# Optimization experiments

Hardware: AMD Instinct MI355X
Metric: run time of the kernel (lower is better)

## Reference

```python
import jax, jax.numpy as jnp
import numpy as np

BIN_AGG = 16  # binAgg in source
K = 3         # forward-default im2col/col2im kernel size


def _im2col(x, k):
    # torch Im2Col (unfold), pad=0, stride=1, dilation=1
    B, C, H, W = x.shape
    oh, ow = H - k + 1, W - k + 1
    patches = [x[:, :, i:i + oh, j:j + ow] for i in range(k) for j in range(k)]
    cols = jnp.stack(patches, axis=2)            # [B, C, k*k, oh, ow]
    return cols.reshape(B, C * k * k, oh * ow)   # [B, C*k*k, L]


def _col2im(cols, k, H, W):
    # torch Col2Im (fold): overlap-add of patches back to [B, C, H, W]
    B, CK, L = cols.shape
    C = CK // (k * k)
    oh = H - k + 1
    cols = cols.reshape(B, C, k, k, oh, oh)
    img = jnp.zeros((B, C, H, W), cols.dtype)
    for i in range(k):
        for j in range(k):
            img = img.at[:, :, i:i + oh, j:j + oh].add(cols[:, :, i, j])
    return img


def bin_active(x):
    # sign(x) scaled by block-wise mean of |x| over blocks of 16 along last dim
    B, Kd, L = x.shape
    blocks = jnp.abs(x).reshape(B, Kd, L // BIN_AGG, BIN_AGG)
    scale = jnp.mean(blocks, axis=-1, keepdims=True)
    scale = jnp.broadcast_to(scale, blocks.shape).reshape(B, Kd, L)
    return scale * jnp.sign(x)


def setup_inputs() -> dict:
    key = jax.random.key(0)
    ks = jax.random.split(key, 5)
    B, Cin, Cout, H = 8, 64, 128, 130
    x = jax.random.normal(ks[0], (B, Cin, H, H), jnp.float32)
    gamma = 1.0 + 0.1 * jax.random.normal(ks[1], (Cin,), jnp.float32)
    beta = 0.1 * jax.random.normal(ks[2], (Cin,), jnp.float32)
    conv_w = 0.05 * jax.random.normal(ks[3], (Cout, Cin, 3, 3), jnp.float32)
    conv_b = 0.05 * jax.random.normal(ks[4], (Cout,), jnp.float32)
    return {"x": x, "gamma": gamma, "beta": beta, "conv_w": conv_w, "conv_b": conv_b}


def reference(x, gamma, beta, conv_w, conv_b):
    eps = 1e-4  # BatchNorm2d eps in source
    # BatchNorm2d (training-mode batch statistics, affine)
    mean = jnp.mean(x, axis=(0, 2, 3), keepdims=True)
    var = jnp.var(x, axis=(0, 2, 3), keepdims=True)
    xbn = (x - mean) * jax.lax.rsqrt(var + eps) * gamma[None, :, None, None] + beta[None, :, None, None]
    H = x.shape[2]
    cols = _im2col(xbn, K)          # [B, C*9, (H-2)^2]
    cols = bin_active(cols)         # block-mean binary quantization
    img = _col2im(cols, K, H, H)    # [B, C, H, W]
    y = jax.lax.conv_general_dilated(
        img, conv_w, window_strides=(1, 1), padding=((1, 1), (1, 1)),
        dimension_numbers=("NCHW", "OIHW", "NCHW"))
    y = y + conv_b[None, :, None, None]
    return jax.nn.relu(y)
```

## Files before the change

### kernel.cpp

```cpp
#include <hip/hip_runtime.h>
#include <math.h>

#define B_    8
#define CIN   64
#define COUT  128
#define H_    130
#define NPIX  (H_*H_)
#define NPX   (B_*NPIX)
#define IMW   132
#define ROWE  (8*IMW*8)

typedef __attribute__((ext_vector_type(8))) short short8;
typedef __attribute__((ext_vector_type(4))) float f32x4;

__device__ __forceinline__ ushort f2bf(float f) {
    uint u = __builtin_bit_cast(uint, f);
    uint r = (u + 0x7FFFu + ((u >> 16) & 1u)) >> 16;
    return (ushort)r;
}

__global__ __launch_bounds__(256) void bn_stage1(
    const float* __restrict__ x, float* __restrict__ part)
{
    const int c = blockIdx.x, b = blockIdx.y, tid = threadIdx.x;
    const float4* p = (const float4*)(x + ((size_t)b*CIN + c)*NPIX);
    float s = 0.f, q = 0.f;
    for (int i = tid; i < NPIX/4; i += 256) {
        float4 v = p[i];
        s += v.x + v.y + v.z + v.w;
        q += v.x*v.x + v.y*v.y + v.z*v.z + v.w*v.w;
    }
    #pragma unroll
    for (int off = 32; off; off >>= 1) { s += __shfl_down(s, off); q += __shfl_down(q, off); }
    __shared__ float ss[4], qq[4];
    if ((tid & 63) == 0) { ss[tid >> 6] = s; qq[tid >> 6] = q; }
    __syncthreads();
    if (tid == 0) {
        s = ss[0] + ss[1] + ss[2] + ss[3];
        q = qq[0] + qq[1] + qq[2] + qq[3];
        part[(c*B_ + b)*2]     = s;
        part[(c*B_ + b)*2 + 1] = q;
    }
}

__global__ void bn_stage2(
    const float* __restrict__ part, const float* __restrict__ gamma,
    const float* __restrict__ beta, float* __restrict__ abuf, float* __restrict__ bbuf)
{
    int c = threadIdx.x;
    float s = 0.f, q = 0.f;
    for (int b = 0; b < B_; ++b) { s += part[(c*B_+b)*2]; q += part[(c*B_+b)*2+1]; }
    float mean = s * (1.0f/135200.f);
    float var  = q * (1.0f/135200.f) - mean*mean;
    float a = gamma[c] / sqrtf(var + 1e-4f);
    abuf[c] = a;
    bbuf[c] = beta[c] - mean * a;
}

__global__ __launch_bounds__(256) void wprep(
    const float* __restrict__ w, ushort* __restrict__ wT)
{
    int i = blockIdx.x*256 + threadIdx.x;
    int co = i / 576, k = i - co*576;
    int dydx = k >> 6, ci = k & 63;
    wT[i] = f2bf(w[co*576 + ci*9 + dydx]);
}

__global__ __launch_bounds__(256) void binfold(
    const float* __restrict__ x, const float* __restrict__ abuf,
    const float* __restrict__ bbuf, ushort* __restrict__ img)
{
    __shared__ __align__(16) ushort tile[H_*66];
    __shared__ float absrow[4][132];
    __shared__ float wsum[4][24];
    const int yy = blockIdx.x;
    const int b  = blockIdx.y;
    const int tid = threadIdx.x, wv = tid >> 6, lane = tid & 63;
    uint* rowU = (uint*)(img + (size_t)(b*IMW + yy)*ROWE);

    if (yy == 0 || yy == IMW-1) {
        for (int i = tid; i < ROWE/2; i += 256) rowU[i] = 0u;
        return;
    }
    const int y = yy - 1;
    const float county = (float)min(min(y + 1, 3), H_ - y);

    for (int it = 0; it < 16; ++it) {
        const int ci = wv*16 + it;
        const float* row = x + (((size_t)b*CIN + ci)*H_ + y)*H_;
        const float a = abuf[ci], bb = bbuf[ci];
        float v0 = a*row[lane]      + bb;
        float v1 = a*row[lane + 64] + bb;
        float v2 = 0.f;
        if (lane < 2) v2 = a*row[lane + 128] + bb;
        absrow[wv][lane]      = fabsf(v0);
        absrow[wv][lane + 64] = fabsf(v1);
        if (lane < 2) absrow[wv][lane + 128] = fabsf(v2);
        asm volatile("s_waitcnt lgkmcnt(0)" ::: "memory");
        if (lane < 24) {
            int j = lane >> 3, bx = lane & 7;
            int s = j + bx*16;
            float acc = 0.f;
            #pragma unroll
            for (int t = 0; t < 16; ++t) acc += absrow[wv][s + t];
            wsum[wv][j*8 + bx] = acc;
        }
        asm volatile("s_waitcnt lgkmcnt(0)" ::: "memory");
        #pragma unroll
        for (int rep = 0; rep < 3; ++rep) {
            int xp = lane + rep*64;
            if (xp < H_) {
                float v = (rep == 0) ? v0 : (rep == 1) ? v1 : v2;
                float sgn = (v > 0.f) ? 1.f : ((v < 0.f) ? -1.f : 0.f);
                float sum = 0.f;
                #pragma unroll
                for (int j = 0; j < 3; ++j) {
                    int ox = xp - j;
                    if ((unsigned)ox < 128u) sum += wsum[wv][j*8 + (ox >> 4)];
                }
                tile[xp*66 + ci] = f2bf(sgn * county * sum * 0.0625f);
            }
        }
    }
    __syncthreads();
    const uint* tU = (const uint*)tile;
    for (int i = tid; i < 8*H_*4; i += 256) {
        int cg = (int)((unsigned)i / 520u);
        int r  = i - cg*520;
        int xp = r >> 2, u = r & 3;
        rowU[(cg*IMW + xp + 1)*4 + u] = tU[xp*33 + cg*4 + u];
    }
    if (tid < 64) {
        int cg = tid >> 3, side = (tid >> 2) & 1, u = tid & 3;
        rowU[(cg*IMW + (side ? (IMW-1) : 0))*4 + u] = 0u;
    }
}

#define LDSE (3*ROWE + 128)
__global__ __launch_bounds__(256, 3) void conv_mfma(
    const ushort* __restrict__ img, const ushort* __restrict__ wT,
    const float* __restrict__ bias, float* __restrict__ out)
{
    __shared__ __align__(16) ushort sB[LDSE];
    const int y = blockIdx.x, b = blockIdx.y;
    const int tid = threadIdx.x, lane = tid & 63, wv = tid >> 6;
    const int l16 = lane & 15, quad = lane >> 4;
    const int ch = wv >> 1, ph = wv & 1;

    {
        const uint4* src = (const uint4*)(img + (size_t)(b*IMW + y)*ROWE);
        uint4* dst = (uint4*)sB;
        for (int i = tid; i < 3*ROWE/8; i += 256) dst[i] = src[i];
    }
    __syncthreads();

    int wIdx[4];
    #pragma unroll
    for (int mt = 0; mt < 4; ++mt)
        wIdx[mt] = (ch*64 + mt*16 + l16)*576 + quad*8;

    const int ldsLane = (quad*IMW + ph*64 + l16)*8;

    f32x4 acc[4][5];
    #pragma unroll
    for (int mt = 0; mt < 4; ++mt)
        #pragma unroll
        for (int nt = 0; nt < 5; ++nt)
            acc[mt][nt] = (f32x4){0.f, 0.f, 0.f, 0.f};

    #pragma unroll 3
    for (int dydx = 0; dydx < 9; ++dydx) {
        const int dy = (int)((unsigned)dydx / 3u);
        const int dx = dydx - dy*3;
        #pragma unroll
        for (int h = 0; h < 2; ++h) {
            short8 af[4], bf[5];
            #pragma unroll
            for (int mt = 0; mt < 4; ++mt)
                af[mt] = *(const short8*)(wT + wIdx[mt] + dydx*64 + h*32);
            const int koff = dy*ROWE + h*4*IMW*8 + dx*8;
            #pragma unroll
            for (int nt = 0; nt < 5; ++nt)
                bf[nt] = *(const short8*)(sB + ldsLane + koff + nt*16*8);
            #pragma unroll
            for (int mt = 0; mt < 4; ++mt)
                #pragma unroll
                for (int nt = 0; nt < 5; ++nt)
                    acc[mt][nt] = __builtin_amdgcn_mfma_f32_16x16x32_bf16(
                        af[mt], bf[nt], acc[mt][nt], 0, 0, 0);
        }
    }

    const size_t ob = (size_t)b*COUT*NPIX + (size_t)y*H_;
    #pragma unroll
    for (int mt = 0; mt < 4; ++mt) {
        #pragma unroll
        for (int r = 0; r < 4; ++r) {
            const int co = ch*64 + mt*16 + quad*4 + r;
            const float bv = bias[co];
            #pragma unroll
            for (int nt = 0; nt < 5; ++nt) {
                int xq = (ph*4 + nt)*16 + l16;
                if (xq < H_) {
                    float v = acc[mt][nt][r] + bv;
                    out[ob + (size_t)co*NPIX + xq] = v > 0.f ? v : 0.f;
                }
            }
        }
    }
}

extern "C" void kernel_launch(void* const* d_in, const int* in_sizes, int n_in,
                              void* d_out, int out_size, void* d_ws, size_t ws_size,
                              hipStream_t stream)
{
    const float* x      = (const float*)d_in[0];
    const float* gamma  = (const float*)d_in[1];
    const float* beta   = (const float*)d_in[2];
    const float* conv_w = (const float*)d_in[3];
    const float* conv_b = (const float*)d_in[4];
    float* out = (float*)d_out;

    float*  part = (float*)d_ws;
    float*  abuf = part + 1024;
    float*  bbuf = abuf + 64;
    ushort* wT   = (ushort*)(bbuf + 64);
    ushort* img  = wT + 73728;

    bn_stage1<<<dim3(CIN, B_), 256, 0, stream>>>(x, part);
    bn_stage2<<<1, 64, 0, stream>>>(part, gamma, beta, abuf, bbuf);
    wprep<<<288, 256, 0, stream>>>(conv_w, wT);
    binfold<<<dim3(IMW, B_), 256, 0, stream>>>(x, abuf, bbuf, img);
    conv_mfma<<<dim3(H_, B_), 256, 0, stream>>>(img, wT, conv_b, out);
}
```

Measured before the change: 194.6 us.

## Merge BN finalize into weight prep, split binfold by channel groups, prefetch conv weights

```diff
diff --git a/kernel.cpp b/kernel.cpp
--- a/kernel.cpp
+++ b/kernel.cpp
@@ -43,59 +43,65 @@
     }
 }
 
-__global__ void bn_stage2(
-    const float* __restrict__ part, const float* __restrict__ gamma,
-    const float* __restrict__ beta, float* __restrict__ abuf, float* __restrict__ bbuf)
-{
-    int c = threadIdx.x;
-    float s = 0.f, q = 0.f;
-    for (int b = 0; b < B_; ++b) { s += part[(c*B_+b)*2]; q += part[(c*B_+b)*2+1]; }
-    float mean = s * (1.0f/135200.f);
-    float var  = q * (1.0f/135200.f) - mean*mean;
-    float a = gamma[c] / sqrtf(var + 1e-4f);
-    abuf[c] = a;
-    bbuf[c] = beta[c] - mean * a;
-}
-
-__global__ __launch_bounds__(256) void wprep(
-    const float* __restrict__ w, ushort* __restrict__ wT)
+__global__ __launch_bounds__(256) void wprep_bn(
+    const float* __restrict__ w, const float* __restrict__ part,
+    const float* __restrict__ gamma, const float* __restrict__ beta,
+    ushort* __restrict__ wT, float* __restrict__ abuf, float* __restrict__ bbuf)
 {
     int i = blockIdx.x*256 + threadIdx.x;
     int co = i / 576, k = i - co*576;
     int dydx = k >> 6, ci = k & 63;
     wT[i] = f2bf(w[co*576 + ci*9 + dydx]);
+    if (blockIdx.x == 0 && threadIdx.x < 64) {
+        int c = threadIdx.x;
+        float s = 0.f, q = 0.f;
+        for (int b = 0; b < B_; ++b) { s += part[(c*B_+b)*2]; q += part[(c*B_+b)*2+1]; }
+        float mean = s * (1.0f/135200.f);
+        float var  = q * (1.0f/135200.f) - mean*mean;
+        float a = gamma[c] / sqrtf(var + 1e-4f);
+        abuf[c] = a;
+        bbuf[c] = beta[c] - mean * a;
+    }
 }
 
 __global__ __launch_bounds__(256) void binfold(
     const float* __restrict__ x, const float* __restrict__ abuf,
     const float* __restrict__ bbuf, ushort* __restrict__ img)
 {
-    __shared__ __align__(16) ushort tile[H_*66];
+    __shared__ __align__(16) ushort tile[H_*18];
     __shared__ float absrow[4][132];
     __shared__ float wsum[4][24];
-    const int yy = blockIdx.x;
-    const int b  = blockIdx.y;
+    const int yy = blockIdx.x, b = blockIdx.y, zg = blockIdx.z;
     const int tid = threadIdx.x, wv = tid >> 6, lane = tid & 63;
     uint* rowU = (uint*)(img + (size_t)(b*IMW + yy)*ROWE);
+    const int cgBase = zg*2;
 
     if (yy == 0 || yy == IMW-1) {
-        for (int i = tid; i < ROWE/2; i += 256) rowU[i] = 0u;
+        for (int i = tid; i < 2*IMW*4; i += 256)
+            rowU[cgBase*IMW*4 + i] = 0u;
         return;
     }
     const int y = yy - 1;
     const float county = (float)min(min(y + 1, 3), H_ - y);
 
-    for (int it = 0; it < 16; ++it) {
-        const int ci = wv*16 + it;
+    const int ci0 = zg*16 + wv*4;
+    float v0[4], v1[4], v2[4];
+    #pragma unroll
+    for (int it = 0; it < 4; ++it) {
+        const int ci = ci0 + it;
         const float* row = x + (((size_t)b*CIN + ci)*H_ + y)*H_;
         const float a = abuf[ci], bb = bbuf[ci];
-        float v0 = a*row[lane]      + bb;
-        float v1 = a*row[lane + 64] + bb;
-        float v2 = 0.f;
-        if (lane < 2) v2 = a*row[lane + 128] + bb;
-        absrow[wv][lane]      = fabsf(v0);
-        absrow[wv][lane + 64] = fabsf(v1);
-        if (lane < 2) absrow[wv][lane + 128] = fabsf(v2);
+        v0[it] = a*row[lane]      + bb;
+        v1[it] = a*row[lane + 64] + bb;
+        v2[it] = (lane < 2) ? (a*row[lane + 128] + bb) : 0.f;
+    }
+
+    #pragma unroll
+    for (int it = 0; it < 4; ++it) {
+        const int cl = wv*4 + it;
+        absrow[wv][lane]      = fabsf(v0[it]);
+        absrow[wv][lane + 64] = fabsf(v1[it]);
+        if (lane < 2) absrow[wv][lane + 128] = fabsf(v2[it]);
         asm volatile("s_waitcnt lgkmcnt(0)" ::: "memory");
         if (lane < 24) {
             int j = lane >> 3, bx = lane & 7;
@@ -110,7 +116,7 @@
         for (int rep = 0; rep < 3; ++rep) {
             int xp = lane + rep*64;
             if (xp < H_) {
-                float v = (rep == 0) ? v0 : (rep == 1) ? v1 : v2;
+                float v = (rep == 0) ? v0[it] : (rep == 1) ? v1[it] : v2[it];
                 float sgn = (v > 0.f) ? 1.f : ((v < 0.f) ? -1.f : 0.f);
                 float sum = 0.f;
                 #pragma unroll
@@ -118,34 +124,32 @@
                     int ox = xp - j;
                     if ((unsigned)ox < 128u) sum += wsum[wv][j*8 + (ox >> 4)];
                 }
-                tile[xp*66 + ci] = f2bf(sgn * county * sum * 0.0625f);
+                tile[xp*18 + cl] = f2bf(sgn * county * sum * 0.0625f);
             }
         }
+        asm volatile("s_waitcnt lgkmcnt(0)" ::: "memory");
     }
     __syncthreads();
     const uint* tU = (const uint*)tile;
-    for (int i = tid; i < 8*H_*4; i += 256) {
-        int cg = (int)((unsigned)i / 520u);
-        int r  = i - cg*520;
-        int xp = r >> 2, u = r & 3;
-        rowU[(cg*IMW + xp + 1)*4 + u] = tU[xp*33 + cg*4 + u];
-    }
-    if (tid < 64) {
-        int cg = tid >> 3, side = (tid >> 2) & 1, u = tid & 3;
+    for (int i = tid; i < H_*8; i += 256) {
+        int xp = i >> 3, p = i & 7;
+        rowU[((cgBase + (p >> 2))*IMW + xp + 1)*4 + (p & 3)] = tU[xp*9 + p];
+    }
+    if (tid < 16) {
+        int cg = cgBase + (tid >> 3), side = (tid >> 2) & 1, u = tid & 3;
         rowU[(cg*IMW + (side ? (IMW-1) : 0))*4 + u] = 0u;
     }
 }
 
-#define LDSE (3*ROWE + 128)
 __global__ __launch_bounds__(256, 3) void conv_mfma(
     const ushort* __restrict__ img, const ushort* __restrict__ wT,
     const float* __restrict__ bias, float* __restrict__ out)
 {
-    __shared__ __align__(16) ushort sB[LDSE];
+    __shared__ __align__(16) ushort sB[3*ROWE];
     const int y = blockIdx.x, b = blockIdx.y;
     const int tid = threadIdx.x, lane = tid & 63, wv = tid >> 6;
     const int l16 = lane & 15, quad = lane >> 4;
-    const int ch = wv >> 1, ph = wv & 1;
+    const int mh = wv >> 1, nh = wv & 1;
 
     {
         const uint4* src = (const uint4*)(img + (size_t)(b*IMW + y)*ROWE);
@@ -154,12 +158,13 @@
     }
     __syncthreads();
 
-    int wIdx[4];
-    #pragma unroll
-    for (int mt = 0; mt < 4; ++mt)
-        wIdx[mt] = (ch*64 + mt*16 + l16)*576 + quad*8;
-
-    const int ldsLane = (quad*IMW + ph*64 + l16)*8;
+    int xBase[5];
+    #pragma unroll
+    for (int nt = 0; nt < 5; ++nt)
+        xBase[nt] = min(nh*80 + nt*16 + l16, 129);
+
+    const ushort* wA = wT + (size_t)(mh*64 + l16)*576 + quad*8;
+    const int bQuad = quad*132;
 
     f32x4 acc[4][5];
     #pragma unroll
@@ -168,27 +173,34 @@
         for (int nt = 0; nt < 5; ++nt)
             acc[mt][nt] = (f32x4){0.f, 0.f, 0.f, 0.f};
 
-    #pragma unroll 3
-    for (int dydx = 0; dydx < 9; ++dydx) {
-        const int dy = (int)((unsigned)dydx / 3u);
-        const int dx = dydx - dy*3;
-        #pragma unroll
-        for (int h = 0; h < 2; ++h) {
-            short8 af[4], bf[5];
+    short8 aCur[4];
+    #pragma unroll
+    for (int mt = 0; mt < 4; ++mt)
+        aCur[mt] = *(const short8*)(wA + mt*16*576);
+
+    #pragma unroll
+    for (int s = 0; s < 18; ++s) {
+        short8 aNxt[4];
+        if (s < 17) {
             #pragma unroll
             for (int mt = 0; mt < 4; ++mt)
-                af[mt] = *(const short8*)(wT + wIdx[mt] + dydx*64 + h*32);
-            const int koff = dy*ROWE + h*4*IMW*8 + dx*8;
+                aNxt[mt] = *(const short8*)(wA + mt*16*576 + (s+1)*32);
+        }
+        const int dydx = s >> 1, h = s & 1;
+        const int dy = dydx / 3, dx = dydx - dy*3;
+        const int gOff = ((dy*8 + h*4)*132 + dx)*8;
+        short8 bf[5];
+        #pragma unroll
+        for (int nt = 0; nt < 5; ++nt)
+            bf[nt] = *(const short8*)(sB + gOff + (bQuad + xBase[nt])*8);
+        #pragma unroll
+        for (int mt = 0; mt < 4; ++mt)
             #pragma unroll
             for (int nt = 0; nt < 5; ++nt)
-                bf[nt] = *(const short8*)(sB + ldsLane + koff + nt*16*8);
-            #pragma unroll
-            for (int mt = 0; mt < 4; ++mt)
-                #pragma unroll
-                for (int nt = 0; nt < 5; ++nt)
-                    acc[mt][nt] = __builtin_amdgcn_mfma_f32_16x16x32_bf16(
-                        af[mt], bf[nt], acc[mt][nt], 0, 0, 0);
-        }
+                acc[mt][nt] = __builtin_amdgcn_mfma_f32_16x16x32_bf16(
+                    aCur[mt], bf[nt], acc[mt][nt], 0, 0, 0);
+        #pragma unroll
+        for (int mt = 0; mt < 4; ++mt) aCur[mt] = aNxt[mt];
     }
 
     const size_t ob = (size_t)b*COUT*NPIX + (size_t)y*H_;
@@ -196,14 +208,14 @@
     for (int mt = 0; mt < 4; ++mt) {
         #pragma unroll
         for (int r = 0; r < 4; ++r) {
-            const int co = ch*64 + mt*16 + quad*4 + r;
+            const int co = mh*64 + mt*16 + quad*4 + r;
             const float bv = bias[co];
             #pragma unroll
             for (int nt = 0; nt < 5; ++nt) {
-                int xq = (ph*4 + nt)*16 + l16;
-                if (xq < H_) {
+                int p = nh*80 + nt*16 + l16;
+                if (p < H_) {
                     float v = acc[mt][nt][r] + bv;
-                    out[ob + (size_t)co*NPIX + xq] = v > 0.f ? v : 0.f;
+                    out[ob + (size_t)co*NPIX + p] = v > 0.f ? v : 0.f;
                 }
             }
         }
@@ -228,8 +240,7 @@
     ushort* img  = wT + 73728;
 
     bn_stage1<<<dim3(CIN, B_), 256, 0, stream>>>(x, part);
-    bn_stage2<<<1, 64, 0, stream>>>(part, gamma, beta, abuf, bbuf);
-    wprep<<<288, 256, 0, stream>>>(conv_w, wT);
-    binfold<<<dim3(IMW, B_), 256, 0, stream>>>(x, abuf, bbuf, img);
+    wprep_bn<<<288, 256, 0, stream>>>(conv_w, part, gamma, beta, wT, abuf, bbuf);
+    binfold<<<dim3(IMW, B_, 4), 256, 0, stream>>>(x, abuf, bbuf, img);
     conv_mfma<<<dim3(H_, B_), 256, 0, stream>>>(img, wT, conv_b, out);
 }
```

Result: no change. 192.2 us (-1.2%).
